# Performance work log

Hardware: AMD Instinct MI355X
Metric: run time of the kernel (lower is better)

Reference implementation:

```python
import jax, jax.numpy as jnp
import numpy as np

B, T, C = 4, 2048, 2048
H, HD = 16, 128  # n_heads, head_dim; C == H*HD


def _rope_rotate(x, cos, sin):
    """x: [b,t,h,d]; cos/sin: [t, d//2]. Complex multiply on interleaved pairs,
    matching torch view_as_complex on reshape(..., -1, 2)."""
    xr = x[..., 0::2]  # real parts  [b,t,h,d/2]
    xi = x[..., 1::2]  # imag parts
    c = cos[None, :, None, :]
    s = sin[None, :, None, :]
    or_ = xr * c - xi * s
    oi_ = xr * s + xi * c
    # interleave back: [..., d/2, 2] -> [..., d]
    return jnp.stack([or_, oi_], axis=-1).reshape(x.shape)


def setup_inputs() -> dict:
    key = jax.random.key(0)
    ks = jax.random.split(key, 6)
    x = jax.random.normal(ks[0], (B, T, C), dtype=jnp.float32)
    # causal boolean mask: True = attend
    attn_mask = jnp.tril(jnp.ones((T, T), dtype=bool))
    # standard RoPE frequencies (theta=10000)
    inv_freq = 1.0 / (10000.0 ** (np.arange(0, HD, 2, dtype=np.float32) / HD))
    ang = np.arange(T, dtype=np.float32)[:, None] * inv_freq[None, :]  # [T, HD/2]
    rope_cos = jnp.asarray(np.cos(ang))
    rope_sin = jnp.asarray(np.sin(ang))
    sc = 1.0 / np.sqrt(C)
    Wq = jax.random.normal(ks[1], (C, C), dtype=jnp.float32) * sc
    Wk = jax.random.normal(ks[2], (C, C), dtype=jnp.float32) * sc
    Wv = jax.random.normal(ks[3], (C, C), dtype=jnp.float32) * sc
    Wp = jax.random.normal(ks[4], (C, C), dtype=jnp.float32) * sc
    return {"x": x, "attn_mask": attn_mask, "rope_cos": rope_cos,
            "rope_sin": rope_sin, "Wq": Wq, "Wk": Wk, "Wv": Wv, "Wp": Wp}


def reference(x, attn_mask, rope_cos, rope_sin, Wq, Wk, Wv, Wp):
    b, t, c = x.shape
    # QKV projections (nn.Linear: y = x @ W.T), reshape to heads
    q = jnp.einsum('btc,dc->btd', x, Wq).reshape(b, t, H, HD)
    k = jnp.einsum('btc,dc->btd', x, Wk).reshape(b, t, H, HD)
    v = jnp.einsum('btc,dc->btd', x, Wv).reshape(b, t, H, HD)
    # RoPE on q, k
    q = _rope_rotate(q, rope_cos[:t], rope_sin[:t])
    k = _rope_rotate(k, rope_cos[:t], rope_sin[:t])
    # SDPA with boolean mask, scale 1/sqrt(head_dim)
    scores = jnp.einsum('bqhd,bkhd->bhqk', q, k) / jnp.sqrt(jnp.asarray(HD, x.dtype))
    neg = jnp.finfo(scores.dtype).min
    scores = jnp.where(attn_mask[None, None, :t, :t], scores, neg)
    attn = jax.nn.softmax(scores, axis=-1)
    out = jnp.einsum('bhqk,bkhd->bqhd', attn, v).reshape(b, t, H * HD)
    return jnp.einsum('btd,cd->btc', out, Wp)
```

## Files before the change

### kernel.cpp

```cpp
#include <hip/hip_runtime.h>

#define B_    4
#define T_    2048
#define C_    2048
#define H_    16
#define HD_   128
#define LDQK  4096

typedef __attribute__((ext_vector_type(8))) short short8v;
typedef __attribute__((ext_vector_type(4))) float float4v;
typedef __attribute__((ext_vector_type(16))) float float16v;

typedef const __attribute__((address_space(1))) void* gld_src_t;
typedef __attribute__((address_space(3))) void* gld_dst_t;
#define GLDS16(g, l) __builtin_amdgcn_global_load_lds((gld_src_t)(g), (gld_dst_t)(l), 16, 0, 0)

__device__ __forceinline__ unsigned short f2bf(float f) {
  unsigned int u = __float_as_uint(f);
  u += 0x7fffu + ((u >> 16) & 1u);
  return (unsigned short)(u >> 16);
}
__device__ __forceinline__ float bf2f(unsigned short s) {
  return __uint_as_float(((unsigned int)s) << 16);
}
__device__ __forceinline__ unsigned int cvtpk_bf16(float lo, float hi) {
  unsigned int r;
  asm("v_cvt_pk_bf16_f32 %0, %1, %2" : "=v"(r) : "v"(lo), "v"(hi));
  return r;
}

__global__ void cvt5_kernel(const float* __restrict__ x,
                            const float* __restrict__ wq, const float* __restrict__ wk,
                            const float* __restrict__ wv, const float* __restrict__ wp,
                            unsigned short* __restrict__ xbf, unsigned short* __restrict__ wdst) {
  int i = blockIdx.x * blockDim.x + threadIdx.x;
  const float4* s;
  ushort4* d;
  if (i < 4194304) {
    s = reinterpret_cast<const float4*>(x) + i;
    d = reinterpret_cast<ushort4*>(xbf) + i;
  } else {
    int j = i - 4194304;
    int w = j >> 20;
    const float* wsrc = (w == 0) ? wq : (w == 1) ? wk : (w == 2) ? wv : wp;
    s = reinterpret_cast<const float4*>(wsrc) + (j & 1048575);
    d = reinterpret_cast<ushort4*>(wdst) + j;
  }
  float4 v = *s;
  ushort4 o;
  o.x = f2bf(v.x); o.y = f2bf(v.y); o.z = f2bf(v.z); o.w = f2bf(v.w);
  *d = o;
}


#define ISSUE_HALF(MAT, HA, KT, CBUF)                                             \
  { const unsigned short* gp_ = (MAT) ? Bm : A;                                   \
    const size_t gb_ = (MAT) ? bbase : abase;                                     \
    _Pragma("unroll")                                                             \
    for (int i_ = 0; i_ < 2; ++i_) {                                              \
      int fo_ = (i_ * 512 + tid) * 16;                              \
      int rl_ = fo_ >> 7;                                            \
      int row_ = (HA) * 128 + rl_;                                                \
      int g_ = (fo_ >> 4) & 7;                                                    \
      int ce_ = ((g_ ^ (rl_ & 7)) << 3);              \
      GLDS16(gp_ + gb_ + (size_t)row_ * K + (KT) * 64 + ce_,                      \
             lds + (CBUF) * 65536 + (MAT) * 32768 + (HA) * 16384 + fo_);          \
    } }

#define RD_A(dst, MI, KK, CBUF)                                                   \
  { int row_ = wm * 128 + (MI) * 16 + lr;                                         \
    dst = *reinterpret_cast<const short8v*>(                                      \
        lds + (CBUF) * 65536 + row_ * 128 + (((KK) * 64 + lg * 16) ^ ((row_ & 7) << 4))); }

#define RD_B(dst, NI, KK, CBUF)                                                   \
  { int row_ = wn * 64 + (NI) * 16 + lr;                                          \
    dst = *reinterpret_cast<const short8v*>(                                      \
        lds + (CBUF) * 65536 + 32768 + row_ * 128 + (((KK) * 64 + lg * 16) ^ ((row_ & 7) << 4))); }

#define MFMA_BLOCK(MBASE, BV)                                                     \
  { __builtin_amdgcn_s_setprio(1);                                                \
    _Pragma("unroll")                                                             \
    for (int ni_ = 0; ni_ < 4; ++ni_) {                                           \
      acc[(MBASE)+0][ni_] = __builtin_amdgcn_mfma_f32_16x16x32_bf16(a0, BV[ni_], acc[(MBASE)+0][ni_], 0,0,0); \
      acc[(MBASE)+1][ni_] = __builtin_amdgcn_mfma_f32_16x16x32_bf16(a1, BV[ni_], acc[(MBASE)+1][ni_], 0,0,0); \
      acc[(MBASE)+2][ni_] = __builtin_amdgcn_mfma_f32_16x16x32_bf16(a2, BV[ni_], acc[(MBASE)+2][ni_], 0,0,0); \
      acc[(MBASE)+3][ni_] = __builtin_amdgcn_mfma_f32_16x16x32_bf16(a3, BV[ni_], acc[(MBASE)+3][ni_], 0,0,0); \
    }                                                                             \
    __builtin_amdgcn_s_setprio(0); }

#define FENCE asm volatile("" ::: "memory")

template<int MODE>
__global__ __launch_bounds__(512, 2)
void gemm256(const unsigned short* __restrict__ A, const unsigned short* __restrict__ Bm,
             void* __restrict__ Cout, unsigned short* __restrict__ vtp,
             int K, int NB, int ldc,
             const float* __restrict__ rc, const float* __restrict__ rs)
{
  extern __shared__ char lds[];
  const int tid = threadIdx.x;
  const int l = tid & 63, w = tid >> 6;
  const int lr = l & 15, lg = l >> 4;
  const int wm = w >> 2, wn = w & 3;

  const int nwg = (int)gridDim.x;
  const int orig = (int)blockIdx.x;
  const int qq = nwg >> 3, rr = nwg & 7;
  const int xcd = orig & 7, idx = orig >> 3;
  const int wg = (xcd < rr ? xcd * (qq + 1) : rr * (qq + 1) + (xcd - rr) * qq) + idx;
  const int bm = wg / NB, bn = wg % NB;

  const size_t abase = (size_t)bm * 256 * (size_t)K;
  const size_t bbase = (size_t)bn * 256 * (size_t)K;

  float4v acc[8][4];
  const float4v fz = {0.f, 0.f, 0.f, 0.f};
#pragma unroll
  for (int i = 0; i < 8; ++i)
#pragma unroll
    for (int j = 0; j < 4; ++j) acc[i][j] = fz;

  const int nk = K >> 6;

  ISSUE_HALF(1, 0, 0, 0)
  ISSUE_HALF(1, 1, 0, 0)
  ISSUE_HALF(0, 0, 0, 0)
  ISSUE_HALF(0, 1, 0, 0)
  asm volatile("s_waitcnt vmcnt(0)" ::: "memory");
  __builtin_amdgcn_s_barrier();
  FENCE;

  short8v a0, a1, a2, a3;
  short8v bv0[4], bv1[4];

  for (int t = 0; t < nk; ++t) {
    const int c = t & 1;

    if (t + 1 < nk) {
      ISSUE_HALF(1, 0, t + 1, c ^ 1)
      ISSUE_HALF(1, 1, t + 1, c ^ 1)
      ISSUE_HALF(0, 0, t + 1, c ^ 1)
      ISSUE_HALF(0, 1, t + 1, c ^ 1)
    }
    FENCE;

    RD_A(a0, 0, 0, c) RD_A(a1, 1, 0, c) RD_A(a2, 2, 0, c) RD_A(a3, 3, 0, c)
    RD_B(bv0[0], 0, 0, c) RD_B(bv0[1], 1, 0, c) RD_B(bv0[2], 2, 0, c) RD_B(bv0[3], 3, 0, c)
    MFMA_BLOCK(0, bv0)
    RD_A(a0, 4, 0, c) RD_A(a1, 5, 0, c) RD_A(a2, 6, 0, c) RD_A(a3, 7, 0, c)
    MFMA_BLOCK(4, bv0)
    RD_A(a0, 0, 1, c) RD_A(a1, 1, 1, c) RD_A(a2, 2, 1, c) RD_A(a3, 3, 1, c)
    RD_B(bv1[0], 0, 1, c) RD_B(bv1[1], 1, 1, c) RD_B(bv1[2], 2, 1, c) RD_B(bv1[3], 3, 1, c)
    MFMA_BLOCK(0, bv1)
    RD_A(a0, 4, 1, c) RD_A(a1, 5, 1, c) RD_A(a2, 6, 1, c) RD_A(a3, 7, 1, c)
    MFMA_BLOCK(4, bv1)

    asm volatile("s_waitcnt vmcnt(0)" ::: "memory");
    __builtin_amdgcn_s_barrier();
    FENCE;
  }

  const int row0 = bm * 256 + wm * 128;
  const int col0 = bn * 256 + wn * 64;
  if (MODE == 3 && bn >= 16) {
#pragma unroll
    for (int mi = 0; mi < 8; ++mi)
#pragma unroll
      for (int ni = 0; ni < 4; ++ni) {
        int vcol = col0 - 4096 + ni * 16 + lr;
        int hh = vcol >> 7, dd = vcol & 127;
        int row = row0 + mi * 16 + lg * 4;
        int bb = row >> 11, t0 = row & 2047;
        ushort4 o4;
        o4.x = f2bf(acc[mi][ni][0]); o4.y = f2bf(acc[mi][ni][1]);
        o4.z = f2bf(acc[mi][ni][2]); o4.w = f2bf(acc[mi][ni][3]);
        *reinterpret_cast<ushort4*>(vtp + (((size_t)(bb * 16 + hh)) << 18) + (((size_t)dd) << 11) + t0) = o4;
      }
  } else if (MODE == 3) {
    const float sgn = (lr & 1) ? 1.0f : -1.0f;
#pragma unroll
    for (int mi = 0; mi < 8; ++mi)
#pragma unroll
      for (int ni = 0; ni < 4; ++ni) {
        int col = col0 + ni * 16 + lr;
        int ii = (col & 127) >> 1;
#pragma unroll
        for (int r2 = 0; r2 < 4; ++r2) {
          int row = row0 + mi * 16 + lg * 4 + r2;
          int tt = row & 2047;
          float v = acc[mi][ni][r2];
          float vp = __shfl_xor(v, 1);
          float cs = rc[tt * 64 + ii];
          float sn = rs[tt * 64 + ii];
          float o = v * cs + sgn * vp * sn;
          ((unsigned short*)Cout)[(size_t)row * ldc + col] = f2bf(o);
        }
      }
  } else {
#pragma unroll
    for (int mi = 0; mi < 8; ++mi)
#pragma unroll
      for (int ni = 0; ni < 4; ++ni)
#pragma unroll
        for (int r2 = 0; r2 < 4; ++r2) {
          int row = row0 + mi * 16 + lg * 4 + r2;
          int col = col0 + ni * 16 + lr;
          ((float*)Cout)[(size_t)row * ldc + col] = acc[mi][ni][r2];
        }
  }
}

__global__ __launch_bounds__(256, 2)
void attn_kernel(const unsigned short* __restrict__ qk,
                 const unsigned short* __restrict__ vt,
                 unsigned short* __restrict__ out)
{
  __shared__ unsigned short Kl[2][64 * 128];
  __shared__ unsigned short Vl[2][128 * 64];

  const int wg = (int)blockIdx.x;
  const int bh = ((wg >> 6) << 3) | (wg & 7);
  const int bx = (wg >> 3) & 7;
  const int b = bh >> 4, h = bh & 15;
  const int tid = threadIdx.x, w = tid >> 6, l = tid & 63;
  const int q32 = l & 31, hi = l >> 5;
  const size_t rowbase = (size_t)b * T_;
  const unsigned short* kbase = qk + rowbase * LDQK + 2048 + h * HD_;
  const unsigned short* vbase = vt + (size_t)bh * (HD_ * (size_t)T_);
  const float SC = 0.12754089f;
  const float16v z16 = {0.f,0.f,0.f,0.f,0.f,0.f,0.f,0.f,0.f,0.f,0.f,0.f,0.f,0.f,0.f,0.f};

#define STAGE(kv0_, bi_)                                                          \
  {                                                                               \
    _Pragma("unroll")                                                             \
    for (int i_ = 0; i_ < 4; ++i_) {                                              \
      int fo = (i_ * 256 + tid) * 16;                                             \
      int row = fo >> 8;                                                          \
      int cb = (fo & 255) ^ ((row & 15) << 4);                                    \
      GLDS16(kbase + (size_t)((kv0_) + row) * LDQK + (cb >> 1), (char*)Kl[bi_] + fo); \
    }                                                                             \
    _Pragma("unroll")                                                             \
    for (int i_ = 0; i_ < 4; ++i_) {                                              \
      int fo = (i_ * 256 + tid) * 16;                                             \
      int r6 = (fo >> 8) & 63;                                                    \
      int s_ = (fo >> 7) & 1;                                                     \
      int dd = r6 | ((s_ ^ ((r6 >> 3) & 1)) << 6);                                \
      int k16 = ((fo >> 4) & 7) ^ (dd & 7);                                       \
      GLDS16(vbase + (size_t)dd * T_ + (kv0_) + k16 * 8, (char*)Vl[bi_] + fo);    \
    }                                                                             \
  }

  for (int sel = 0; sel < 2; ++sel) {
    const int qt = sel ? bx : (15 - bx);
    const int q0w = qt * 128 + w * 32;
    const int qg = q0w + q32;

    short8v qf[8];
#pragma unroll
    for (int kf = 0; kf < 8; ++kf) {
      short8v t = *reinterpret_cast<const short8v*>(
          qk + (rowbase + q0w + q32) * (size_t)LDQK + h * HD_ + kf * 16 + hi * 8);
      short8v r;
#pragma unroll
      for (int e = 0; e < 8; ++e) r[e] = (short)f2bf(bf2f((unsigned short)t[e]) * SC);
      qf[kf] = r;
    }

    float16v o[4];
#pragma unroll
    for (int db = 0; db < 4; ++db) o[db] = z16;
    float m_run = -1e30f, lsum = 0.f;

    const int nkv = 2 * (qt + 1);

    STAGE(0, 0);
    __syncthreads();

    for (int tile = 0; tile < nkv; ++tile) {
      const int kv0 = tile * 64;
      const int bi = tile & 1;
      if (tile + 1 < nkv) STAGE((tile + 1) * 64, bi ^ 1);

      if (kv0 <= q0w + 31) {
        float16v stv[2];
        stv[0] = z16; stv[1] = z16;
        __builtin_amdgcn_s_setprio(1);
#pragma unroll
        for (int kb = 0; kb < 2; ++kb) {
          int key = kb * 32 + q32;
          int swz = (key & 15) << 4;
          int rbase = key * 256;
#pragma unroll
          for (int kf = 0; kf < 8; ++kf) {
            short8v ak = *reinterpret_cast<const short8v*>(
                (char*)Kl[bi] + rbase + ((kf * 32 + hi * 16) ^ swz));
            stv[kb] = __builtin_amdgcn_mfma_f32_32x32x16_bf16(ak, qf[kf], stv[kb], 0, 0, 0);
          }
        }
        __builtin_amdgcn_s_setprio(0);
        if (kv0 + 63 > q0w) {
#pragma unroll
          for (int kb = 0; kb < 2; ++kb)
#pragma unroll
            for (int r = 0; r < 16; ++r) {
              int key = kv0 + kb * 32 + (r & 3) + 8 * ((r >> 2) & 3) + 4 * hi;
              if (key > qg) stv[kb][r] = -1e30f;
            }
        }
        float t16[16];
#pragma unroll
        for (int r = 0; r < 16; ++r) t16[r] = fmaxf(stv[0][r], stv[1][r]);
#pragma unroll
        for (int s = 8; s >= 1; s >>= 1)
#pragma unroll
          for (int r = 0; r < s; ++r) t16[r] = fmaxf(t16[r], t16[r + s]);
        float pm = fmaxf(t16[0], __shfl_xor(t16[0], 32));

        if (!__all(pm <= m_run + 8.0f)) {
          float mn = fmaxf(m_run, pm);
          float fac = exp2f(m_run - mn);
          lsum *= fac;
          m_run = mn;
#pragma unroll
          for (int r = 0; r < 16; ++r) {
            int src = (r & 3) + 8 * ((r >> 2) & 3) + 4 * hi;
            float fr = __shfl(fac, src);
#pragma unroll
            for (int db = 0; db < 4; ++db) o[db][r] *= fr;
          }
        }
        {
          float s16[16];
#pragma unroll
          for (int r = 0; r < 16; ++r) {
            float p0 = exp2f(stv[0][r] - m_run);
            float p1 = exp2f(stv[1][r] - m_run);
            stv[0][r] = p0; stv[1][r] = p1;
            s16[r] = p0 + p1;
          }
#pragma unroll
          for (int s = 8; s >= 1; s >>= 1)
#pragma unroll
            for (int r = 0; r < s; ++r) s16[r] += s16[r + s];
          lsum += s16[0] + __shfl_xor(s16[0], 32);
        }
        unsigned int pw0[8], pw1[8], xw0[8], xw1[8];
#pragma unroll
        for (int j = 0; j < 8; ++j) {
          pw0[j] = cvtpk_bf16(stv[0][2 * j], stv[0][2 * j + 1]);
          pw1[j] = cvtpk_bf16(stv[1][2 * j], stv[1][2 * j + 1]);
        }
#pragma unroll
        for (int j = 0; j < 8; ++j) {
          xw0[j] = __shfl_xor(pw0[j], 32);
          xw1[j] = __shfl_xor(pw1[j], 32);
        }
        union UW { unsigned int u[4]; short8v v; };
        short8v pb[4];
        {
          UW a0, a1, c0, c1;
          a0.u[0] = hi ? xw0[2] : pw0[0];  a0.u[1] = hi ? xw0[3] : pw0[1];
          a0.u[2] = hi ? pw0[2] : xw0[0];  a0.u[3] = hi ? pw0[3] : xw0[1];
          a1.u[0] = hi ? xw0[6] : pw0[4];  a1.u[1] = hi ? xw0[7] : pw0[5];
          a1.u[2] = hi ? pw0[6] : xw0[4];  a1.u[3] = hi ? pw0[7] : xw0[5];
          c0.u[0] = hi ? xw1[2] : pw1[0];  c0.u[1] = hi ? xw1[3] : pw1[1];
          c0.u[2] = hi ? pw1[2] : xw1[0];  c0.u[3] = hi ? pw1[3] : xw1[1];
          c1.u[0] = hi ? xw1[6] : pw1[4];  c1.u[1] = hi ? xw1[7] : pw1[5];
          c1.u[2] = hi ? pw1[6] : xw1[4];  c1.u[3] = hi ? pw1[7] : xw1[5];
          pb[0] = a0.v; pb[1] = a1.v; pb[2] = c0.v; pb[3] = c1.v;
        }
        __builtin_amdgcn_s_setprio(1);
#pragma unroll
        for (int db = 0; db < 4; ++db) {
          int dd = db * 32 + q32;
          int rb2 = (dd & 63) * 256 + ((((dd >> 6) ^ ((dd >> 3) & 1)) & 1) << 7);
          int swz = (dd & 7) << 4;
#pragma unroll
          for (int kb16 = 0; kb16 < 4; ++kb16) {
            short8v bv = *reinterpret_cast<const short8v*>(
                (char*)Vl[bi] + rb2 + ((kb16 * 32 + hi * 16) ^ swz));
            o[db] = __builtin_amdgcn_mfma_f32_32x32x16_bf16(pb[kb16], bv, o[db], 0, 0, 0);
          }
        }
        __builtin_amdgcn_s_setprio(0);
      }
      __syncthreads();
    }

    float linv = 1.0f / lsum;
#pragma unroll
    for (int r = 0; r < 16; ++r) {
      int src = (r & 3) + 8 * ((r >> 2) & 3) + 4 * hi;
      float lr_ = __shfl(linv, src);
      size_t rowoff = (rowbase + q0w + src) * (size_t)C_ + h * HD_ + q32;
#pragma unroll
      for (int db = 0; db < 4; ++db)
        out[rowoff + db * 32] = f2bf(o[db][r] * lr_);
    }
  }
#undef STAGE
}

extern "C" void kernel_launch(void* const* d_in, const int* in_sizes, int n_in,
                              void* d_out, int out_size, void* d_ws, size_t ws_size,
                              hipStream_t stream) {
  (void)in_sizes; (void)n_in; (void)out_size; (void)ws_size;
  const float* x  = (const float*)d_in[0];
  const float* rc = (const float*)d_in[2];
  const float* rs = (const float*)d_in[3];
  const float* Wq = (const float*)d_in[4];
  const float* Wk = (const float*)d_in[5];
  const float* Wv = (const float*)d_in[6];
  const float* Wp = (const float*)d_in[7];
  float* outp = (float*)d_out;

  unsigned short* ws    = (unsigned short*)d_ws;
  unsigned short* x_bf  = ws;
  unsigned short* wqkv  = x_bf + 16777216;
  unsigned short* wp_bf = wqkv + 12582912;
  unsigned short* qkbuf = wp_bf + 4194304;
  unsigned short* vtbuf = qkbuf + 33554432;
  unsigned short* ao    = x_bf;

  hipFuncSetAttribute((const void*)gemm256<0>, hipFuncAttributeMaxDynamicSharedMemorySize, 131072);
  hipFuncSetAttribute((const void*)gemm256<3>, hipFuncAttributeMaxDynamicSharedMemorySize, 131072);

  cvt5_kernel<<<32768, 256, 0, stream>>>(x, Wq, Wk, Wv, Wp, x_bf, wqkv);

  gemm256<3><<<dim3(768), 512, 131072, stream>>>(x_bf, wqkv, qkbuf, vtbuf, 2048, 24, 4096, rc, rs);

  attn_kernel<<<dim3(512), 256, 0, stream>>>(qkbuf, vtbuf, ao);

  gemm256<0><<<dim3(256), 512, 131072, stream>>>(ao, wp_bf, outp, nullptr, 2048, 8, 2048, nullptr, nullptr);
}
```

Before: 414.7 us.

## Software-pipeline LDS fragment reads across the K-loop barrier in GEMM

Restructures the GEMM main loop to double-buffer register fragments: the first A/B fragments for the next K tile are read from LDS right after the barrier, and the last MFMA block runs after the barrier so LDS reads overlap matrix-core work. It also removes the setprio calls and compiler memory fences, and adds an explicit lgkmcnt wait plus a sched_barrier before the global-load wait. The aim is to hide LDS read latency and barrier stalls behind MFMAs. In exchange it uses more VGPRs, which at 512 threads with two blocks per CU could cause spills or lower occupancy.

```diff
diff --git a/kernel.cpp b/kernel.cpp
--- a/kernel.cpp
+++ b/kernel.cpp
@@ -77,18 +77,13 @@
     dst = *reinterpret_cast<const short8v*>(                                      \
         lds + (CBUF) * 65536 + 32768 + row_ * 128 + (((KK) * 64 + lg * 16) ^ ((row_ & 7) << 4))); }
 
-#define MFMA_BLOCK(MBASE, BV)                                                     \
-  { __builtin_amdgcn_s_setprio(1);                                                \
+#define MFMA16(MB, AV, BV)                                                        \
     _Pragma("unroll")                                                             \
     for (int ni_ = 0; ni_ < 4; ++ni_) {                                           \
-      acc[(MBASE)+0][ni_] = __builtin_amdgcn_mfma_f32_16x16x32_bf16(a0, BV[ni_], acc[(MBASE)+0][ni_], 0,0,0); \
-      acc[(MBASE)+1][ni_] = __builtin_amdgcn_mfma_f32_16x16x32_bf16(a1, BV[ni_], acc[(MBASE)+1][ni_], 0,0,0); \
-      acc[(MBASE)+2][ni_] = __builtin_amdgcn_mfma_f32_16x16x32_bf16(a2, BV[ni_], acc[(MBASE)+2][ni_], 0,0,0); \
-      acc[(MBASE)+3][ni_] = __builtin_amdgcn_mfma_f32_16x16x32_bf16(a3, BV[ni_], acc[(MBASE)+3][ni_], 0,0,0); \
-    }                                                                             \
-    __builtin_amdgcn_s_setprio(0); }
-
-#define FENCE asm volatile("" ::: "memory")
+      _Pragma("unroll")                                                           \
+      for (int mi_ = 0; mi_ < 4; ++mi_)                                           \
+        acc[(MB)+mi_][ni_] = __builtin_amdgcn_mfma_f32_16x16x32_bf16(AV[mi_], BV[ni_], acc[(MB)+mi_][ni_], 0,0,0); \
+    }
 
 template<int MODE>
 __global__ __launch_bounds__(512, 2)
@@ -128,10 +123,10 @@
   ISSUE_HALF(0, 1, 0, 0)
   asm volatile("s_waitcnt vmcnt(0)" ::: "memory");
   __builtin_amdgcn_s_barrier();
-  FENCE;
-
-  short8v a0, a1, a2, a3;
-  short8v bv0[4], bv1[4];
+
+  short8v aC[4], aN[4], bC[4], bN[4];
+  RD_A(aC[0], 0, 0, 0) RD_A(aC[1], 1, 0, 0) RD_A(aC[2], 2, 0, 0) RD_A(aC[3], 3, 0, 0)
+  RD_B(bC[0], 0, 0, 0) RD_B(bC[1], 1, 0, 0) RD_B(bC[2], 2, 0, 0) RD_B(bC[3], 3, 0, 0)
 
   for (int t = 0; t < nk; ++t) {
     const int c = t & 1;
@@ -142,22 +137,28 @@
       ISSUE_HALF(0, 0, t + 1, c ^ 1)
       ISSUE_HALF(0, 1, t + 1, c ^ 1)
     }
-    FENCE;
-
-    RD_A(a0, 0, 0, c) RD_A(a1, 1, 0, c) RD_A(a2, 2, 0, c) RD_A(a3, 3, 0, c)
-    RD_B(bv0[0], 0, 0, c) RD_B(bv0[1], 1, 0, c) RD_B(bv0[2], 2, 0, c) RD_B(bv0[3], 3, 0, c)
-    MFMA_BLOCK(0, bv0)
-    RD_A(a0, 4, 0, c) RD_A(a1, 5, 0, c) RD_A(a2, 6, 0, c) RD_A(a3, 7, 0, c)
-    MFMA_BLOCK(4, bv0)
-    RD_A(a0, 0, 1, c) RD_A(a1, 1, 1, c) RD_A(a2, 2, 1, c) RD_A(a3, 3, 1, c)
-    RD_B(bv1[0], 0, 1, c) RD_B(bv1[1], 1, 1, c) RD_B(bv1[2], 2, 1, c) RD_B(bv1[3], 3, 1, c)
-    MFMA_BLOCK(0, bv1)
-    RD_A(a0, 4, 1, c) RD_A(a1, 5, 1, c) RD_A(a2, 6, 1, c) RD_A(a3, 7, 1, c)
-    MFMA_BLOCK(4, bv1)
-
+
+    RD_A(aN[0], 4, 0, c) RD_A(aN[1], 5, 0, c) RD_A(aN[2], 6, 0, c) RD_A(aN[3], 7, 0, c)
+    MFMA16(0, aC, bC)
+
+    RD_A(aC[0], 0, 1, c) RD_A(aC[1], 1, 1, c) RD_A(aC[2], 2, 1, c) RD_A(aC[3], 3, 1, c)
+    RD_B(bN[0], 0, 1, c) RD_B(bN[1], 1, 1, c) RD_B(bN[2], 2, 1, c) RD_B(bN[3], 3, 1, c)
+    MFMA16(4, aN, bC)
+
+    RD_A(aN[0], 4, 1, c) RD_A(aN[1], 5, 1, c) RD_A(aN[2], 6, 1, c) RD_A(aN[3], 7, 1, c)
+    MFMA16(0, aC, bN)
+
+    asm volatile("s_waitcnt lgkmcnt(0)" ::: "memory");
+    __builtin_amdgcn_sched_barrier(0);
     asm volatile("s_waitcnt vmcnt(0)" ::: "memory");
     __builtin_amdgcn_s_barrier();
-    FENCE;
+
+    MFMA16(4, aN, bN)
+
+    if (t + 1 < nk) {
+      RD_A(aC[0], 0, 0, c ^ 1) RD_A(aC[1], 1, 0, c ^ 1) RD_A(aC[2], 2, 0, c ^ 1) RD_A(aC[3], 3, 0, c ^ 1)
+      RD_B(bC[0], 0, 0, c ^ 1) RD_B(bC[1], 1, 0, c ^ 1) RD_B(bC[2], 2, 0, c ^ 1) RD_B(bC[3], 3, 0, c ^ 1)
+    }
   }
 
   const int row0 = bm * 256 + wm * 128;
```

After: 403.0 us, median of 2. -2.8%, faster.
